# Optimization experiments

Measured on AMD Instinct MI355X. Metric: run time of the kernel, lower is better.

The kernel has to match this reference:

```python
import jax, jax.numpy as jnp
import numpy as np

LAMBDA_SMOOTHNESS = 1.0
NUM_NODES = 100000
NUM_EDGES = 320000
D_FEAT = 256
NUM_GRAPHS = 128
NUM_CLASSES = 10


def setup_inputs() -> dict:
    key = jax.random.key(0)
    k1, k2, k3, k4, k5 = jax.random.split(key, 5)
    logits = jax.random.normal(k1, (NUM_GRAPHS, NUM_CLASSES), dtype=jnp.float32)
    labels = jax.random.randint(k2, (NUM_GRAPHS,), 0, NUM_CLASSES, dtype=jnp.int64)
    x = jax.random.normal(k3, (NUM_NODES, D_FEAT), dtype=jnp.float32)
    edge_index = jax.random.randint(k4, (2, NUM_EDGES), 0, NUM_NODES, dtype=jnp.int64)
    batch = jnp.sort(jax.random.randint(k5, (NUM_NODES,), 0, NUM_GRAPHS, dtype=jnp.int64))
    return {"logits": logits, "labels": labels, "x": x,
            "edge_index": edge_index, "batch": batch}


def reference(logits, labels, x, edge_index, batch):
    # --- cross entropy over graphs (mean reduction, like F.cross_entropy) ---
    logp = jax.nn.log_softmax(logits, axis=-1)
    ce_loss = -jnp.mean(jnp.take_along_axis(logp, labels[:, None], axis=1))

    # --- Dirichlet smoothness energy, vectorized over all graphs ---
    num_graphs = (jnp.max(batch) + 1).astype(x.dtype)
    row, col = edge_index[0], edge_index[1]
    # edges crossing graph boundaries are dropped by the per-graph edge_mask
    within = (batch[row] == batch[col]).astype(x.dtype)  # [E]
    # per-node degree counting only within-graph edges (== per-graph degree)
    deg = jax.ops.segment_sum(within, row, num_segments=x.shape[0])  # [N]
    deg_inv_sqrt = jnp.where(deg > 0, deg ** -0.5, jnp.zeros_like(deg))
    norm = deg_inv_sqrt[row] * deg_inv_sqrt[col] * within  # [E]
    diff = x[row] - x[col]  # [E, D]
    energy = jnp.sum(norm * jnp.sum(diff * diff, axis=-1))
    smoothness_loss = energy / num_graphs

    return ce_loss + LAMBDA_SMOOTHNESS * smoothness_loss
```

## Files before the change

kernel.cpp:

```cpp
#include <hip/hip_runtime.h>
#include <math.h>

__global__ __launch_bounds__(256) void deg_ce_mask_kernel(
        const int* __restrict__ row, const int* __restrict__ col,
        const int* __restrict__ batch, unsigned int* __restrict__ deg,
        unsigned long long* __restrict__ mask, int E, int nWaves,
        const float* __restrict__ logits, const int* __restrict__ labels,
        float* __restrict__ out, int G, int C) {
    int gtid = blockIdx.x * blockDim.x + threadIdx.x;
    int lane = threadIdx.x & 63;
    int w = gtid >> 6;

    bool hit = false;
    if (gtid < E) {
        int r = row[gtid], c = col[gtid];
        if (batch[r] == batch[c]) {
            hit = true;
            atomicAdd(&deg[r], 1u);
        }
    }
    unsigned long long m = __ballot(hit);
    if (lane == 0 && w < nWaves) mask[w] = m;

    if (blockIdx.x == 0) {
        __shared__ float sh[128];
        int g = threadIdx.x;
        if (g < 128) {
            float lp = 0.f;
            if (g < G) {
                const float* lg = logits + (size_t)g * C;
                float mx = lg[0];
                for (int d = 1; d < C; ++d) mx = fmaxf(mx, lg[d]);
                float s = 0.f;
                for (int d = 0; d < C; ++d) s += expf(lg[d] - mx);
                lp = lg[labels[g]] - mx - logf(s);
            }
            sh[g] = lp;
        }
        __syncthreads();
        for (int o = 64; o > 0; o >>= 1) {
            if (threadIdx.x < o) sh[threadIdx.x] += sh[threadIdx.x + o];
            __syncthreads();
        }
        if (threadIdx.x == 0) out[0] = (float)(-(double)sh[0] / (double)G);
    }
}

__global__ __launch_bounds__(256) void energy_kernel(
        const float* __restrict__ x,
        const int* __restrict__ row, const int* __restrict__ col,
        const unsigned int* __restrict__ deg,
        const unsigned long long* __restrict__ mask,
        const int* __restrict__ batch,
        float* __restrict__ out, int E, int D4, int N, int nWaves) {
    int gtid = blockIdx.x * blockDim.x + threadIdx.x;
    int wave = gtid >> 6;
    int lane = threadIdx.x & 63;
    int wv = threadIdx.x >> 6;

    double wsum = 0.0;
    unsigned long long m = (wave < nWaves) ? mask[wave] : 0ULL;
    if (m) {
        int e = wave * 64 + lane;
        bool bit = (m >> lane) & 1ULL;
        int r = 0, c = 0;
        float norm = 0.f;
        bool hit = false;
        if (bit) {
            r = row[e];
            c = col[e];
            unsigned int dr = deg[r];
            unsigned int dc = deg[c];
            if (dc > 0u) {
                float ir = 1.0f / sqrtf((float)dr);
                float ic = 1.0f / sqrtf((float)dc);
                norm = ir * ic;
                hit = true;
            }
        }
        unsigned long long bm = __ballot(hit);
        while (bm) {
            int src = __ffsll((unsigned long long)bm) - 1;
            bm &= bm - 1;
            int rr = __shfl(r, src);
            int cc = __shfl(c, src);
            float nn = __shfl(norm, src);
            const float4 a = ((const float4*)(x + (size_t)rr * (size_t)(D4 * 4)))[lane];
            const float4 b = ((const float4*)(x + (size_t)cc * (size_t)(D4 * 4)))[lane];
            float dx = a.x - b.x, dy = a.y - b.y, dz = a.z - b.z, dw = a.w - b.w;
            float ss = dx * dx + dy * dy + dz * dz + dw * dw;
            #pragma unroll
            for (int o = 32; o > 0; o >>= 1) ss += __shfl_xor(ss, o);
            if (lane == 0) wsum += (double)(nn * ss);
        }
    }

    __shared__ double sdw[4];
    if (lane == 0) sdw[wv] = wsum;
    __syncthreads();
    if (threadIdx.x == 0) {
        double bsum = sdw[0] + sdw[1] + sdw[2] + sdw[3];
        if (bsum != 0.0) {
            double ng = (double)(batch[N - 1] + 1);
            atomicAdd(out, (float)(bsum / ng));
        }
    }
}

extern "C" void kernel_launch(void* const* d_in, const int* in_sizes, int n_in,
                              void* d_out, int out_size, void* d_ws, size_t ws_size,
                              hipStream_t stream) {
    const float* logits = (const float*)d_in[0];
    const int* labels = (const int*)d_in[1];
    const float* x = (const float*)d_in[2];
    const int* edge_index = (const int*)d_in[3];
    const int* batch = (const int*)d_in[4];

    const int C = 10;
    const int G = in_sizes[0] / C;
    const int E = in_sizes[3] / 2;
    const int N = in_sizes[4];
    const int D = in_sizes[2] / N;
    const int D4 = D / 4;

    const int* row = edge_index;
    const int* col = edge_index + E;

    int nWaves = (E + 63) / 64;

    size_t off = 0;
    unsigned int* deg = (unsigned int*)((char*)d_ws + off); off += (size_t)N * 4;
    off = (off + 15) & ~(size_t)15;
    unsigned long long* mask = (unsigned long long*)((char*)d_ws + off);

    float* out = (float*)d_out;

    hipMemsetAsync(deg, 0, (size_t)N * 4, stream);

    int degBlocks = (E + 255) / 256;
    deg_ce_mask_kernel<<<degBlocks, 256, 0, stream>>>(
        row, col, batch, deg, mask, E, nWaves, logits, labels, out, G, C);

    int eBlocks = (nWaves + 3) / 4;
    energy_kernel<<<eBlocks, 256, 0, stream>>>(
        x, row, col, deg, mask, batch, out, E, D4, N, nWaves);
}
```

Baseline: 19.94 us.

## Compact batch ids to bytes and process four edges per thread

Replaces the deg memset with an init kernel that zeroes deg and writes a uint8 copy of batch, folding in the cross-entropy computation. The degree/mask kernel then loads row and col as int4, so each thread handles four edges and gathers from the smaller byte-sized batch array. The mask is stored as four interleaved bit planes per wave, and the energy kernel walks those planes in one wave. This shrinks the random-gather footprint and the number of threads. The byte-sized batch copy is only correct when there are at most 256 graphs.

```diff
diff --git a/kernel.cpp b/kernel.cpp
--- a/kernel.cpp
+++ b/kernel.cpp
@@ -1,26 +1,26 @@
 #include <hip/hip_runtime.h>
 #include <math.h>
 
-__global__ __launch_bounds__(256) void deg_ce_mask_kernel(
-        const int* __restrict__ row, const int* __restrict__ col,
-        const int* __restrict__ batch, unsigned int* __restrict__ deg,
-        unsigned long long* __restrict__ mask, int E, int nWaves,
+__global__ __launch_bounds__(256) void k0_init_ce(
+        unsigned int* __restrict__ deg, unsigned char* __restrict__ batch8,
+        const int* __restrict__ batch, int N,
         const float* __restrict__ logits, const int* __restrict__ labels,
         float* __restrict__ out, int G, int C) {
-    int gtid = blockIdx.x * blockDim.x + threadIdx.x;
-    int lane = threadIdx.x & 63;
-    int w = gtid >> 6;
-
-    bool hit = false;
-    if (gtid < E) {
-        int r = row[gtid], c = col[gtid];
-        if (batch[r] == batch[c]) {
-            hit = true;
-            atomicAdd(&deg[r], 1u);
-        }
+    int tid = blockIdx.x * blockDim.x + threadIdx.x;
+    int nthreads = gridDim.x * blockDim.x;
+    int N4 = N >> 2;
+    for (int i = tid; i < N4; i += nthreads) {
+        ((uint4*)deg)[i] = make_uint4(0u, 0u, 0u, 0u);
+        int4 b4 = ((const int4*)batch)[i];
+        uchar4 p;
+        p.x = (unsigned char)b4.x; p.y = (unsigned char)b4.y;
+        p.z = (unsigned char)b4.z; p.w = (unsigned char)b4.w;
+        ((uchar4*)batch8)[i] = p;
     }
-    unsigned long long m = __ballot(hit);
-    if (lane == 0 && w < nWaves) mask[w] = m;
+    for (int i = (N4 << 2) + tid; i < N; i += nthreads) {
+        deg[i] = 0u;
+        batch8[i] = (unsigned char)batch[i];
+    }
 
     if (blockIdx.x == 0) {
         __shared__ float sh[128];
@@ -46,52 +46,94 @@
     }
 }
 
-__global__ __launch_bounds__(256) void energy_kernel(
+__global__ __launch_bounds__(256) void k1_deg_mask(
+        const int* __restrict__ row, const int* __restrict__ col,
+        const unsigned char* __restrict__ batch8,
+        unsigned int* __restrict__ deg,
+        unsigned long long* __restrict__ mask, int E, int T4, int nW) {
+    int t = blockIdx.x * blockDim.x + threadIdx.x;
+    int lane = threadIdx.x & 63;
+    int w = t >> 6;
+
+    int4 r4 = make_int4(0, 0, 0, 0), c4 = make_int4(0, 0, 0, 0);
+    if (t < T4) {
+        r4 = ((const int4*)row)[t];
+        c4 = ((const int4*)col)[t];
+    }
+    int rr[4] = { r4.x, r4.y, r4.z, r4.w };
+    int cc[4] = { c4.x, c4.y, c4.z, c4.w };
+
+    bool h[4];
+    #pragma unroll
+    for (int j = 0; j < 4; ++j) {
+        int e = (t << 2) + j;
+        h[j] = (t < T4) && (e < E) && (batch8[rr[j]] == batch8[cc[j]]);
+        if (h[j]) atomicAdd(&deg[rr[j]], 1u);
+    }
+    #pragma unroll
+    for (int j = 0; j < 4; ++j) {
+        unsigned long long b = __ballot(h[j]);
+        if (lane == 0 && w < nW) mask[(w << 2) + j] = b;
+    }
+}
+
+__global__ __launch_bounds__(256) void k2_energy(
         const float* __restrict__ x,
         const int* __restrict__ row, const int* __restrict__ col,
         const unsigned int* __restrict__ deg,
         const unsigned long long* __restrict__ mask,
         const int* __restrict__ batch,
-        float* __restrict__ out, int E, int D4, int N, int nWaves) {
+        float* __restrict__ out, int D4, int N, int nW) {
     int gtid = blockIdx.x * blockDim.x + threadIdx.x;
     int wave = gtid >> 6;
     int lane = threadIdx.x & 63;
     int wv = threadIdx.x >> 6;
 
     double wsum = 0.0;
-    unsigned long long m = (wave < nWaves) ? mask[wave] : 0ULL;
-    if (m) {
-        int e = wave * 64 + lane;
-        bool bit = (m >> lane) & 1ULL;
-        int r = 0, c = 0;
-        float norm = 0.f;
-        bool hit = false;
-        if (bit) {
-            r = row[e];
-            c = col[e];
-            unsigned int dr = deg[r];
-            unsigned int dc = deg[c];
-            if (dc > 0u) {
-                float ir = 1.0f / sqrtf((float)dr);
-                float ic = 1.0f / sqrtf((float)dc);
-                norm = ir * ic;
-                hit = true;
+    if (wave < nW) {
+        unsigned long long m0 = mask[(wave << 2) + 0];
+        unsigned long long m1 = mask[(wave << 2) + 1];
+        unsigned long long m2 = mask[(wave << 2) + 2];
+        unsigned long long m3 = mask[(wave << 2) + 3];
+        unsigned long long planes[4] = { m0, m1, m2, m3 };
+        if (m0 | m1 | m2 | m3) {
+            #pragma unroll
+            for (int j = 0; j < 4; ++j) {
+                unsigned long long m = planes[j];
+                if (!m) continue;
+                int e = (((wave << 6) + lane) << 2) + j;
+                bool bit = (m >> lane) & 1ULL;
+                int r = 0, c = 0;
+                float norm = 0.f;
+                bool hit = false;
+                if (bit) {
+                    r = row[e];
+                    c = col[e];
+                    unsigned int dr = deg[r];
+                    unsigned int dc = deg[c];
+                    if (dc > 0u) {
+                        float ir = 1.0f / sqrtf((float)dr);
+                        float ic = 1.0f / sqrtf((float)dc);
+                        norm = ir * ic;
+                        hit = true;
+                    }
+                }
+                unsigned long long bm = __ballot(hit);
+                while (bm) {
+                    int src = __ffsll((unsigned long long)bm) - 1;
+                    bm &= bm - 1;
+                    int rs = __shfl(r, src);
+                    int cs = __shfl(c, src);
+                    float nn = __shfl(norm, src);
+                    const float4 a = ((const float4*)(x + (size_t)rs * (size_t)(D4 * 4)))[lane];
+                    const float4 b = ((const float4*)(x + (size_t)cs * (size_t)(D4 * 4)))[lane];
+                    float dx = a.x - b.x, dy = a.y - b.y, dz = a.z - b.z, dw = a.w - b.w;
+                    float ss = dx * dx + dy * dy + dz * dz + dw * dw;
+                    #pragma unroll
+                    for (int o = 32; o > 0; o >>= 1) ss += __shfl_xor(ss, o);
+                    if (lane == 0) wsum += (double)(nn * ss);
+                }
             }
-        }
-        unsigned long long bm = __ballot(hit);
-        while (bm) {
-            int src = __ffsll((unsigned long long)bm) - 1;
-            bm &= bm - 1;
-            int rr = __shfl(r, src);
-            int cc = __shfl(c, src);
-            float nn = __shfl(norm, src);
-            const float4 a = ((const float4*)(x + (size_t)rr * (size_t)(D4 * 4)))[lane];
-            const float4 b = ((const float4*)(x + (size_t)cc * (size_t)(D4 * 4)))[lane];
-            float dx = a.x - b.x, dy = a.y - b.y, dz = a.z - b.z, dw = a.w - b.w;
-            float ss = dx * dx + dy * dy + dz * dz + dw * dw;
-            #pragma unroll
-            for (int o = 32; o > 0; o >>= 1) ss += __shfl_xor(ss, o);
-            if (lane == 0) wsum += (double)(nn * ss);
         }
     }
 
@@ -126,22 +168,25 @@
     const int* row = edge_index;
     const int* col = edge_index + E;
 
-    int nWaves = (E + 63) / 64;
+    int T4 = (E + 3) / 4;
+    int nW = (T4 + 63) / 64;
 
     size_t off = 0;
     unsigned int* deg = (unsigned int*)((char*)d_ws + off); off += (size_t)N * 4;
+    unsigned char* batch8 = (unsigned char*)((char*)d_ws + off); off += (size_t)N;
     off = (off + 15) & ~(size_t)15;
     unsigned long long* mask = (unsigned long long*)((char*)d_ws + off);
 
     float* out = (float*)d_out;
 
-    hipMemsetAsync(deg, 0, (size_t)N * 4, stream);
+    k0_init_ce<<<128, 256, 0, stream>>>(deg, batch8, batch, N,
+                                        logits, labels, out, G, C);
 
-    int degBlocks = (E + 255) / 256;
-    deg_ce_mask_kernel<<<degBlocks, 256, 0, stream>>>(
-        row, col, batch, deg, mask, E, nWaves, logits, labels, out, G, C);
+    int k1Blocks = (T4 + 255) / 256;
+    k1_deg_mask<<<k1Blocks, 256, 0, stream>>>(row, col, batch8, deg,
+                                              mask, E, T4, nW);
 
-    int eBlocks = (nWaves + 3) / 4;
-    energy_kernel<<<eBlocks, 256, 0, stream>>>(
-        x, row, col, deg, mask, batch, out, E, D4, N, nWaves);
+    int k2Blocks = (nW + 3) / 4;
+    k2_energy<<<k2Blocks, 256, 0, stream>>>(x, row, col, deg, mask, batch,
+                                            out, D4, N, nW);
 }
```

Result: no change. 19.72 us (median of 2 runs) (-1.1%).
